# Optimization experiments

Hardware: AMD Instinct MI355X
Metric: run time of the kernel (lower is better)

The kernel has to match this reference:

```python
import jax, jax.numpy as jnp
import numpy as np

N, T, DM = 8192, 32, 128   # nodes, patches, d_model (d_in = T*DM = 4096)
M, NNZ = 1024, 131072      # hyperedges, incidences
EPS = 1e-5
SLOPE = 0.2


def _bn(x, g, b, axes):
    # BatchNorm with batch statistics (training-mode math, eval dropout)
    m = jnp.mean(x, axis=axes, keepdims=True)
    v = jnp.var(x, axis=axes, keepdims=True)
    return (x - m) / jnp.sqrt(v + EPS) * g + b


def _hconv(x, he_attr, he_n, he_e, W, att, bias, heads):
    # PyG HypergraphConv, use_attention=True, attention_mode='node', concat=False
    out = W.shape[1] // heads
    xt = (x @ W).reshape(N, heads, out)          # [N, H, F]
    et = (he_attr @ W).reshape(M, heads, out)    # [M, H, F]
    xi = xt[he_n]                                # [nnz, H, F] gather node feats
    ej = et[he_e]                                # [nnz, H, F] gather edge feats
    alpha = jnp.sum(jnp.concatenate([xi, ej], axis=-1) * att, axis=-1)  # [nnz, H]
    alpha = jax.nn.leaky_relu(alpha, SLOPE)
    # segment softmax grouped by hyperedge (attention_mode='node')
    amax = jax.ops.segment_max(alpha, he_e, num_segments=M)
    ex = jnp.exp(alpha - amax[he_e])
    alpha = ex / jax.ops.segment_sum(ex, he_e, num_segments=M)[he_e]
    # degree normalizers (hyperedge_weight == 1)
    ones = jnp.ones((NNZ,), x.dtype)
    Dn = jax.ops.segment_sum(ones, he_n, num_segments=N)
    Dinv = jnp.where(Dn > 0, 1.0 / Dn, 0.0)
    Bm = jax.ops.segment_sum(ones, he_e, num_segments=M)
    Binv = jnp.where(Bm > 0, 1.0 / Bm, 0.0)
    # node -> edge, then edge -> node message passing
    eo = jax.ops.segment_sum(alpha[:, :, None] * Binv[he_e][:, None, None] * xi,
                             he_e, num_segments=M)                     # [M, H, F]
    no = jax.ops.segment_sum(alpha[:, :, None] * Dinv[he_n][:, None, None] * eo[he_e],
                             he_n, num_segments=N)                     # [N, H, F]
    return no.mean(axis=1) + bias  # concat=False -> mean over heads


def setup_inputs() -> dict:
    key = jax.random.key(0)
    ks = jax.random.split(key, 16)
    d_in = T * DM
    s = 0.02
    inp = {
        "x": jax.random.normal(ks[0], (N, T, DM), jnp.float32),
        "he_nodes": jax.random.randint(ks[1], (NNZ,), 0, N),
        "he_edges": jax.random.randint(ks[2], (NNZ,), 0, M),
        "W1": jax.random.normal(ks[3], (d_in, DM), jnp.float32) * s,
        "b1": jnp.zeros((DM,), jnp.float32),
        "g1": jnp.ones((DM,), jnp.float32), "be1": jnp.zeros((DM,), jnp.float32),
        "Wh1": jax.random.normal(ks[4], (DM, 4 * DM), jnp.float32) * s,
        "att1": jax.random.normal(ks[5], (1, 4, 2 * DM), jnp.float32) * s,
        "bh1": jnp.zeros((DM,), jnp.float32),
        "g2": jnp.ones((DM,), jnp.float32), "be2": jnp.zeros((DM,), jnp.float32),
        "Wh2": jax.random.normal(ks[6], (DM, DM), jnp.float32) * s,
        "att2": jax.random.normal(ks[7], (1, 1, 2 * DM), jnp.float32) * s,
        "bh2": jnp.zeros((DM,), jnp.float32),
        "g3": jnp.ones((DM,), jnp.float32), "be3": jnp.zeros((DM,), jnp.float32),
        "W3": jax.random.normal(ks[8], (DM, d_in), jnp.float32) * s,
        "b3": jnp.zeros((d_in,), jnp.float32),
        "g4": jnp.ones((DM,), jnp.float32), "be4": jnp.zeros((DM,), jnp.float32),
    }
    return inp


def reference(x, he_nodes, he_edges, W1, b1, g1, be1, Wh1, att1, bh1,
              g2, be2, Wh2, att2, bh2, g3, be3, W3, b3, g4, be4):
    src = x
    h = x.reshape(N, T * DM)
    h = jax.nn.leaky_relu(h @ W1 + b1, SLOPE)
    h = _bn(h, g1, be1, 0)
    # hyperedge_attr = incidence^T @ h  (== to_dense_adj(...).T @ h)
    he_attr = jax.ops.segment_sum(h[he_nodes], he_edges, num_segments=M)
    h = h + _hconv(h, he_attr, he_nodes, he_edges, Wh1, att1, bh1, 4)
    h = _bn(h, g2, be2, 0)
    he_attr = jax.ops.segment_sum(h[he_nodes], he_edges, num_segments=M)
    h = h + _hconv(h, he_attr, he_nodes, he_edges, Wh2, att2, bh2, 1)
    h = _bn(h, g3, be3, 0)
    h = jax.nn.leaky_relu(h @ W3 + b3, SLOPE)
    h = src + h.reshape(N, T, DM)
    h = _bn(h, g4, be4, (0, 1))  # BN over channel DM, stats over (N, T)
    return h
```

## Files before the change

kernel.cpp:

```cpp
#include <hip/hip_runtime.h>
#include <hip/hip_bf16.h>
#include <math.h>

#define NN   8192
#define TT   32
#define DIN  4096
#define MME  1024
#define NNZK 131072
#define EPSV 1e-5f
#define MALL (NN + MME)

typedef __attribute__((ext_vector_type(8))) short bf16x8;
typedef __attribute__((ext_vector_type(4))) float f32x4;

__device__ __forceinline__ float lrelu(float v){ return v > 0.f ? v : 0.2f*v; }
__device__ __forceinline__ short f2b(float f){
    union { __hip_bfloat16 h; short s; } u; u.h = __float2bfloat16(f); return u.s;
}

__global__ void zero_i(int* p, int n){ int i = blockIdx.x*256 + threadIdx.x; if (i < n) p[i] = 0; }
__global__ void zero_f(float* p, int n){ int i = blockIdx.x*256 + threadIdx.x; if (i < n) p[i] = 0.f; }
__global__ void copy_i(const int* a, int* b, int n){ int i = blockIdx.x*256 + threadIdx.x; if (i < n) b[i] = a[i]; }

__global__ void count_seg(const int* __restrict__ he_n, const int* __restrict__ he_e,
                          int* __restrict__ ncnt, int* __restrict__ ecnt){
    int k = blockIdx.x*256 + threadIdx.x;
    if (k < NNZK){ atomicAdd(&ecnt[he_e[k]], 1); atomicAdd(&ncnt[he_n[k]], 1); }
}

__global__ void scan_excl(const int* __restrict__ cnt, int* __restrict__ off, int n){
    __shared__ int buf[1024];
    __shared__ int carry;
    int t = threadIdx.x;
    if (t == 0) carry = 0;
    __syncthreads();
    for (int base = 0; base < n; base += 1024){
        int i = base + t;
        int v = (i < n) ? cnt[i] : 0;
        buf[t] = v; __syncthreads();
        for (int s = 1; s < 1024; s <<= 1){
            int tmp = (t >= s) ? buf[t - s] : 0;
            __syncthreads();
            buf[t] += tmp;
            __syncthreads();
        }
        if (i < n) off[i] = carry + buf[t] - v;
        __syncthreads();
        if (t == 1023) carry += buf[1023];
        __syncthreads();
    }
    if (t == 0) off[n] = carry;
}

__global__ void fill_perm(const int* __restrict__ seg, int* __restrict__ cur, int* __restrict__ perm){
    int k = blockIdx.x*256 + threadIdx.x;
    if (k < NNZK){ int p = atomicAdd(&cur[seg[k]], 1); perm[p] = k; }
}

__global__ void wconv_t(const float* __restrict__ W, __hip_bfloat16* __restrict__ BT, int K, int N){
    __shared__ float tile[32][33];
    int k0 = blockIdx.y*32, n0 = blockIdx.x*32;
    int tx = threadIdx.x & 31, ty = threadIdx.x >> 5;
    for (int i = ty; i < 32; i += 8) tile[i][tx] = W[(size_t)(k0+i)*N + n0+tx];
    __syncthreads();
    for (int i = ty; i < 32; i += 8)
        BT[(size_t)(n0+i)*K + k0 + tx] = __float2bfloat16(tile[tx][i]);
}

#define SWZ(b) ((b) ^ ((((b) >> 6) & 7) << 4))

template<int EPI>
__global__ __launch_bounds__(256) void gemm_mfma(
    const float* __restrict__ A, const __hip_bfloat16* __restrict__ BT,
    float* __restrict__ C, const float* __restrict__ bias, const float* __restrict__ add,
    float* __restrict__ slots, int M, int N, int K, int kchunk)
{
    __shared__ f32x4 AsRaw[512];
    __shared__ f32x4 BsRaw[512];
    char* As = (char*)AsRaw;
    char* Bs = (char*)BsRaw;
    const int tid = threadIdx.x;
    const int lane = tid & 63;
    const int w = tid >> 6;
    const int m0 = blockIdx.y << 7, n0 = blockIdx.x << 7;
    const int kz = blockIdx.z * kchunk;
    const int wr = (w >> 1) << 6, wc = (w & 1) << 6;

    const int s0 = tid, s1 = tid + 256;
    const int r0 = s0 >> 2, k0b = (s0 & 3) << 3;
    const int r1 = s1 >> 2, k1b = (s1 & 3) << 3;
    const float* pA0 = A + (size_t)(m0 + r0)*K + kz + k0b;
    const float* pA1 = A + (size_t)(m0 + r1)*K + kz + k1b;
    const __hip_bfloat16* pB0 = BT + (size_t)(n0 + r0)*K + kz + k0b;
    const __hip_bfloat16* pB1 = BT + (size_t)(n0 + r1)*K + kz + k1b;
    const int wo0 = SWZ(s0 << 4), wo1 = SWZ(s1 << 4);

    int raOff[4], rbOff[4];
#pragma unroll
    for (int f = 0; f < 4; f++){
        int rowA = wr + f*16 + (lane & 15);
        raOff[f] = SWZ(rowA*64 + ((lane >> 4) << 4));
        int rowB = wc + f*16 + (lane & 15);
        rbOff[f] = SWZ(rowB*64 + ((lane >> 4) << 4));
    }

    f32x4 acc[4][4] = {};

    float4 a0l = *(const float4*)pA0, a0h = *(const float4*)(pA0+4);
    float4 a1l = *(const float4*)pA1, a1h = *(const float4*)(pA1+4);
    bf16x8 b0 = *(const bf16x8*)pB0, b1 = *(const bf16x8*)pB1;

    const int nsteps = kchunk >> 5;
    for (int ks = 0; ks < nsteps; ks++){
        bf16x8 va0, va1;
        va0[0]=f2b(a0l.x); va0[1]=f2b(a0l.y); va0[2]=f2b(a0l.z); va0[3]=f2b(a0l.w);
        va0[4]=f2b(a0h.x); va0[5]=f2b(a0h.y); va0[6]=f2b(a0h.z); va0[7]=f2b(a0h.w);
        va1[0]=f2b(a1l.x); va1[1]=f2b(a1l.y); va1[2]=f2b(a1l.z); va1[3]=f2b(a1l.w);
        va1[4]=f2b(a1h.x); va1[5]=f2b(a1h.y); va1[6]=f2b(a1h.z); va1[7]=f2b(a1h.w);
        __syncthreads();
        *(bf16x8*)(As + wo0) = va0;
        *(bf16x8*)(As + wo1) = va1;
        *(bf16x8*)(Bs + wo0) = b0;
        *(bf16x8*)(Bs + wo1) = b1;
        __syncthreads();
        if (ks + 1 < nsteps){
            pA0 += 32; pA1 += 32; pB0 += 32; pB1 += 32;
            a0l = *(const float4*)pA0; a0h = *(const float4*)(pA0+4);
            a1l = *(const float4*)pA1; a1h = *(const float4*)(pA1+4);
            b0 = *(const bf16x8*)pB0;  b1 = *(const bf16x8*)pB1;
        }
        bf16x8 af[4], bfr[4];
#pragma unroll
        for (int f = 0; f < 4; f++){
            af[f]  = *(const bf16x8*)(As + raOff[f]);
            bfr[f] = *(const bf16x8*)(Bs + rbOff[f]);
        }
#pragma unroll
        for (int mf = 0; mf < 4; mf++)
#pragma unroll
            for (int nf = 0; nf < 4; nf++)
                acc[mf][nf] = __builtin_amdgcn_mfma_f32_16x16x32_bf16(af[mf], bfr[nf], acc[mf][nf], 0, 0, 0);
    }

    if (EPI == 2){
        __shared__ float sS[128], sQ[128];
        if (tid < 128){ sS[tid] = 0.f; sQ[tid] = 0.f; }
        __syncthreads();
#pragma unroll
        for (int nf = 0; nf < 4; nf++){
            int lc = wc + nf*16 + (lane & 15);
            int col = n0 + lc;
            float bv = bias[col];
            float s = 0.f, q = 0.f;
#pragma unroll
            for (int mf = 0; mf < 4; mf++){
#pragma unroll
                for (int r = 0; r < 4; r++){
                    int row = m0 + wr + mf*16 + ((lane >> 4) << 2) + r;
                    float v = acc[mf][nf][r] + bv;
                    v = lrelu(v);
                    v += add[(size_t)row*N + col];
                    C[(size_t)row*N + col] = v;
                    s += v; q += v*v;
                }
            }
            atomicAdd(&sS[lc], s);
            atomicAdd(&sQ[lc], q);
        }
        __syncthreads();
        if (tid < 128){
            atomicAdd(&slots[blockIdx.x*256 + tid], sS[tid]);
            atomicAdd(&slots[blockIdx.x*256 + 128 + tid], sQ[tid]);
        }
    } else {
        float* Cz = C + (size_t)blockIdx.z * ((size_t)M * (size_t)N);
#pragma unroll
        for (int mf = 0; mf < 4; mf++){
#pragma unroll
            for (int nf = 0; nf < 4; nf++){
                int col = n0 + wc + nf*16 + (lane & 15);
#pragma unroll
                for (int r = 0; r < 4; r++){
                    int row = m0 + wr + mf*16 + ((lane >> 4) << 2) + r;
                    Cz[(size_t)row*N + col] = acc[mf][nf][r];
                }
            }
        }
    }
}

__global__ void reduce8s(const float* __restrict__ part, const float* __restrict__ bias,
                         float* __restrict__ out, int nf4, int parts, float* __restrict__ slots){
    int tid = threadIdx.x;
    int i = blockIdx.x*256 + tid;
    float4 s = ((const float4*)part)[i];
    for (int z = 1; z < parts; z++){
        float4 p = ((const float4*)part)[(size_t)z*nf4 + i];
        s.x += p.x; s.y += p.y; s.z += p.z; s.w += p.w;
    }
    int c0 = (i & 31) << 2;
    s.x = lrelu(s.x + bias[c0+0]); s.y = lrelu(s.y + bias[c0+1]);
    s.z = lrelu(s.z + bias[c0+2]); s.w = lrelu(s.w + bias[c0+3]);
    ((float4*)out)[i] = s;
    __shared__ float S[128], Q[128];
    if (tid < 128){ S[tid] = 0.f; Q[tid] = 0.f; }
    __syncthreads();
    atomicAdd(&S[c0+0], s.x); atomicAdd(&Q[c0+0], s.x*s.x);
    atomicAdd(&S[c0+1], s.y); atomicAdd(&Q[c0+1], s.y*s.y);
    atomicAdd(&S[c0+2], s.z); atomicAdd(&Q[c0+2], s.z*s.z);
    atomicAdd(&S[c0+3], s.w); atomicAdd(&Q[c0+3], s.w*s.w);
    __syncthreads();
    if (tid < 128){
        int slot = blockIdx.x & 31;
        atomicAdd(&slots[slot*256 + tid], S[tid]);
        atomicAdd(&slots[slot*256 + 128 + tid], Q[tid]);
    }
}

__global__ void bn_stats_v2(const float* __restrict__ x, float* __restrict__ slots, int rows){
    int cg = threadIdx.x & 31, rg = threadIdx.x >> 5;
    float4 s = {0,0,0,0}, q = {0,0,0,0};
    for (int r = blockIdx.x*8 + rg; r < rows; r += gridDim.x*8){
        float4 v = ((const float4*)x)[(size_t)r*32 + cg];
        s.x += v.x; q.x += v.x*v.x;
        s.y += v.y; q.y += v.y*v.y;
        s.z += v.z; q.z += v.z*v.z;
        s.w += v.w; q.w += v.w*v.w;
    }
    __shared__ float S[128], Q[128];
    if (threadIdx.x < 128){ S[threadIdx.x] = 0.f; Q[threadIdx.x] = 0.f; }
    __syncthreads();
    int c0 = cg << 2;
    atomicAdd(&S[c0+0], s.x); atomicAdd(&Q[c0+0], q.x);
    atomicAdd(&S[c0+1], s.y); atomicAdd(&Q[c0+1], q.y);
    atomicAdd(&S[c0+2], s.z); atomicAdd(&Q[c0+2], q.z);
    atomicAdd(&S[c0+3], s.w); atomicAdd(&Q[c0+3], q.w);
    __syncthreads();
    if (threadIdx.x < 128){
        int slot = blockIdx.x & 31;
        atomicAdd(&slots[slot*256 + threadIdx.x], S[threadIdx.x]);
        atomicAdd(&slots[slot*256 + 128 + threadIdx.x], Q[threadIdx.x]);
    }
}

__global__ void bn_finalize2(const float* __restrict__ slots, int nslots,
                             const float* __restrict__ g, const float* __restrict__ b,
                             float invR, float* __restrict__ coef){
    int c = threadIdx.x;
    float s = 0.f, q = 0.f;
    for (int k = 0; k < nslots; k++){ s += slots[k*256 + c]; q += slots[k*256 + 128 + c]; }
    float m = s*invR;
    float v = q*invR - m*m;
    float sc = g[c]*rsqrtf(v + EPSV);
    coef[c] = sc;
    coef[128 + c] = b[c] - m*sc;
}

__global__ void bn_apply4(float4* __restrict__ x, const float* __restrict__ coef, size_t n4){
    size_t i = (size_t)blockIdx.x*blockDim.x + threadIdx.x;
    size_t stride = (size_t)gridDim.x*blockDim.x;
    for (; i < n4; i += stride){
        int c0 = (int)(i & 31) * 4;
        float4 v = x[i];
        v.x = v.x*coef[c0+0] + coef[128+c0+0];
        v.y = v.y*coef[c0+1] + coef[128+c0+1];
        v.z = v.z*coef[c0+2] + coef[128+c0+2];
        v.w = v.w*coef[c0+3] + coef[128+c0+3];
        x[i] = v;
    }
}

__global__ void seg_sum_edge(const int* __restrict__ eoff, const int* __restrict__ eperm,
                             const int* __restrict__ he_n, const float* __restrict__ h,
                             float* __restrict__ out){
    int m = blockIdx.x, c = threadIdx.x;
    int s0 = eoff[m], cnt = eoff[m+1] - s0;
    __shared__ int sn[128];
    float acc = 0.f;
    for (int base = 0; base < cnt; base += 128){
        int i = base + c;
        if (i < cnt) sn[c] = he_n[eperm[s0+i]];
        __syncthreads();
        int lim = min(128, cnt - base);
        for (int j = 0; j < lim; j++) acc += h[(size_t)sn[j]*128 + c];
        __syncthreads();
    }
    out[(size_t)m*128 + c] = acc;
}

template<int H>
__global__ void row_att(const float* __restrict__ xt, const float* __restrict__ att,
                        int aoff, float* __restrict__ out){
    int n = blockIdx.x, lane = threadIdx.x;
#pragma unroll
    for (int h = 0; h < H; h++){
        const float* xr = xt + (size_t)n*(H*128) + h*128;
        const float* ar = att + h*256 + aoff;
        float s = xr[lane]*ar[lane] + xr[lane+64]*ar[lane+64];
        for (int d = 32; d > 0; d >>= 1) s += __shfl_down(s, d);
        if (lane == 0) out[n*H + h] = s;
    }
}

template<int H>
__global__ void seg_softmax(const int* __restrict__ eoff, const int* __restrict__ eperm,
                            const int* __restrict__ he_n,
                            const float* __restrict__ ax, const float* __restrict__ ae,
                            float* __restrict__ alpha){
    int m = blockIdx.x, t = threadIdx.x;
    int s0 = eoff[m], cnt = eoff[m+1] - s0;
    if (cnt == 0) return;
    __shared__ float red[128];
    float aeh[H];
#pragma unroll
    for (int h = 0; h < H; h++) aeh[h] = ae[m*H + h];
    float lmax[H];
#pragma unroll
    for (int h = 0; h < H; h++) lmax[h] = -1e30f;
    for (int i = t; i < cnt; i += 128){
        int k = eperm[s0+i]; int n = he_n[k];
#pragma unroll
        for (int h = 0; h < H; h++){
            float v = lrelu(ax[n*H + h] + aeh[h]);
            alpha[(size_t)k*H + h] = v;
            lmax[h] = fmaxf(lmax[h], v);
        }
    }
    float gmax[H];
#pragma unroll
    for (int h = 0; h < H; h++){
        red[t] = lmax[h]; __syncthreads();
        for (int s = 64; s > 0; s >>= 1){ if (t < s) red[t] = fmaxf(red[t], red[t+s]); __syncthreads(); }
        gmax[h] = red[0]; __syncthreads();
    }
    float lsum[H];
#pragma unroll
    for (int h = 0; h < H; h++) lsum[h] = 0.f;
    for (int i = t; i < cnt; i += 128){
        int k = eperm[s0+i];
#pragma unroll
        for (int h = 0; h < H; h++){
            float ex = __expf(alpha[(size_t)k*H + h] - gmax[h]);
            alpha[(size_t)k*H + h] = ex;
            lsum[h] += ex;
        }
    }
    float ginv[H];
#pragma unroll
    for (int h = 0; h < H; h++){
        red[t] = lsum[h]; __syncthreads();
        for (int s = 64; s > 0; s >>= 1){ if (t < s) red[t] += red[t+s]; __syncthreads(); }
        ginv[h] = 1.f/red[0]; __syncthreads();
    }
    for (int i = t; i < cnt; i += 128){
        int k = eperm[s0+i];
#pragma unroll
        for (int h = 0; h < H; h++) alpha[(size_t)k*H + h] *= ginv[h];
    }
}

__global__ void seg_eo4(const int* __restrict__ eoff, const int* __restrict__ eperm,
                        const int* __restrict__ he_n,
                        const float* __restrict__ alpha, const float* __restrict__ xt,
                        float* __restrict__ eo){
    int m = blockIdx.x;
    int c = threadIdx.x & 127, hb = threadIdx.x >> 7;
    int s0 = eoff[m], cnt = eoff[m+1] - s0;
    __shared__ int sn[128];
    __shared__ float sa[128][4];
    float acc0 = 0.f, acc1 = 0.f;
    for (int base = 0; base < cnt; base += 128){
        int i = base + threadIdx.x;
        if (threadIdx.x < 128 && i < cnt){
            int k = eperm[s0+i];
            sn[threadIdx.x] = he_n[k];
#pragma unroll
            for (int h = 0; h < 4; h++) sa[threadIdx.x][h] = alpha[(size_t)k*4 + h];
        }
        __syncthreads();
        int lim = min(128, cnt - base);
        for (int j = 0; j < lim; j++){
            const float* xr = xt + (size_t)sn[j]*512;
            acc0 += sa[j][hb]   * xr[hb*128 + c];
            acc1 += sa[j][hb+2] * xr[(hb+2)*128 + c];
        }
        __syncthreads();
    }
    float binv = cnt > 0 ? 1.f/(float)cnt : 0.f;
    eo[(size_t)m*512 + hb*128 + c]     = acc0*binv;
    eo[(size_t)m*512 + (hb+2)*128 + c] = acc1*binv;
}

__global__ void seg_eo1(const int* __restrict__ eoff, const int* __restrict__ eperm,
                        const int* __restrict__ he_n,
                        const float* __restrict__ alpha, const float* __restrict__ xt,
                        float* __restrict__ eo){
    int m = blockIdx.x, c = threadIdx.x;
    int s0 = eoff[m], cnt = eoff[m+1] - s0;
    __shared__ int sn[128];
    __shared__ float sa[128];
    float acc = 0.f;
    for (int base = 0; base < cnt; base += 128){
        int i = base + c;
        if (i < cnt){
            int k = eperm[s0+i];
            sn[c] = he_n[k];
            sa[c] = alpha[k];
        }
        __syncthreads();
        int lim = min(128, cnt - base);
        for (int j = 0; j < lim; j++) acc += sa[j]*xt[(size_t)sn[j]*128 + c];
        __syncthreads();
    }
    float binv = cnt > 0 ? 1.f/(float)cnt : 0.f;
    eo[(size_t)m*128 + c] = acc*binv;
}

template<int H>
__global__ void seg_node_out(const int* __restrict__ noff, const int* __restrict__ nperm,
                             const int* __restrict__ he_e,
                             const float* __restrict__ alpha, const float* __restrict__ eo,
                             const float* __restrict__ hin, const float* __restrict__ bias,
                             float* __restrict__ hout){
    int n = blockIdx.x, c = threadIdx.x;
    int s0 = noff[n], cnt = noff[n+1] - s0;
    float acc = 0.f;
    for (int i = 0; i < cnt; i++){
        int k = nperm[s0+i]; int e = he_e[k];
        const float* er = eo + (size_t)e*(128*H);
#pragma unroll
        for (int h = 0; h < H; h++) acc += alpha[(size_t)k*H + h]*er[h*128 + c];
    }
    float dinv = cnt > 0 ? 1.f/((float)cnt*(float)H) : 0.f;
    hout[(size_t)n*128 + c] = hin[(size_t)n*128 + c] + bias[c] + acc*dinv;
}

extern "C" void kernel_launch(void* const* d_in, const int* in_sizes, int n_in,
                              void* d_out, int out_size, void* d_ws, size_t ws_size,
                              hipStream_t stream){
    const float* x    = (const float*)d_in[0];
    const int*   he_n = (const int*)  d_in[1];
    const int*   he_e = (const int*)  d_in[2];
    const float* W1   = (const float*)d_in[3];
    const float* b1   = (const float*)d_in[4];
    const float* g1   = (const float*)d_in[5];
    const float* be1  = (const float*)d_in[6];
    const float* Wh1  = (const float*)d_in[7];
    const float* att1 = (const float*)d_in[8];
    const float* bh1  = (const float*)d_in[9];
    const float* g2   = (const float*)d_in[10];
    const float* be2  = (const float*)d_in[11];
    const float* Wh2  = (const float*)d_in[12];
    const float* att2 = (const float*)d_in[13];
    const float* bh2  = (const float*)d_in[14];
    const float* g3   = (const float*)d_in[15];
    const float* be3  = (const float*)d_in[16];
    const float* W3   = (const float*)d_in[17];
    const float* b3   = (const float*)d_in[18];
    const float* g4   = (const float*)d_in[19];
    const float* be4  = (const float*)d_in[20];
    float* out = (float*)d_out;

    char* ws = (char*)d_ws;
    size_t off = 0;
    auto alloc = [&](size_t bytes)->char*{ char* p = ws + off; off += (bytes + 255) & ~(size_t)255; return p; };

    float* hall1  = (float*)alloc((size_t)MALL*128*4);
    float* hall2  = (float*)alloc((size_t)MALL*128*4);
    float* h3     = (float*)alloc((size_t)NN*128*4);
    float* xt1    = (float*)alloc((size_t)MALL*512*4);
    float* xt2    = (float*)alloc((size_t)MALL*128*4);
    float* eo     = (float*)alloc((size_t)MME*512*4);
    float* alpha  = (float*)alloc((size_t)NNZK*4*4);
    float* ax     = (float*)alloc((size_t)NN*4*4);
    float* ae     = (float*)alloc((size_t)MME*4*4);
    float* slots  = (float*)alloc((size_t)32*256*4);
    float* coef   = (float*)alloc(256*4);
    float* part   = (float*)alloc((size_t)8*NN*128*4);
    __hip_bfloat16* W1T  = (__hip_bfloat16*)alloc((size_t)128*DIN*2);
    __hip_bfloat16* Wh1T = (__hip_bfloat16*)alloc((size_t)512*128*2);
    __hip_bfloat16* Wh2T = (__hip_bfloat16*)alloc((size_t)128*128*2);
    __hip_bfloat16* W3T  = (__hip_bfloat16*)alloc((size_t)DIN*128*2);
    int* ecnt  = (int*)alloc(MME*4);
    int* eoffb = (int*)alloc((MME+1)*4);
    int* ecur  = (int*)alloc(MME*4);
    int* ncnt  = (int*)alloc(NN*4);
    int* noffb = (int*)alloc((NN+1)*4);
    int* ncur  = (int*)alloc(NN*4);
    int* eperm = (int*)alloc((size_t)NNZK*4);
    int* nperm = (int*)alloc((size_t)NNZK*4);

    zero_i<<<(MME+255)/256, 256, 0, stream>>>(ecnt, MME);
    zero_i<<<(NN+255)/256, 256, 0, stream>>>(ncnt, NN);
    count_seg<<<NNZK/256, 256, 0, stream>>>(he_n, he_e, ncnt, ecnt);
    scan_excl<<<1, 1024, 0, stream>>>(ecnt, eoffb, MME);
    scan_excl<<<1, 1024, 0, stream>>>(ncnt, noffb, NN);
    copy_i<<<(MME+255)/256, 256, 0, stream>>>(eoffb, ecur, MME);
    copy_i<<<(NN+255)/256, 256, 0, stream>>>(noffb, ncur, NN);
    fill_perm<<<NNZK/256, 256, 0, stream>>>(he_e, ecur, eperm);
    fill_perm<<<NNZK/256, 256, 0, stream>>>(he_n, ncur, nperm);

    wconv_t<<<dim3(128/32, DIN/32), 256, 0, stream>>>(W1,  W1T,  DIN, 128);
    wconv_t<<<dim3(512/32, 128/32), 256, 0, stream>>>(Wh1, Wh1T, 128, 512);
    wconv_t<<<dim3(128/32, 128/32), 256, 0, stream>>>(Wh2, Wh2T, 128, 128);
    wconv_t<<<dim3(DIN/32, 128/32), 256, 0, stream>>>(W3,  W3T,  128, DIN);

    gemm_mfma<0><<<dim3(1, NN/128, 8), 256, 0, stream>>>(x, W1T, part, nullptr, nullptr, nullptr, NN, 128, DIN, DIN/8);
    zero_f<<<32, 256, 0, stream>>>(slots, 32*256);
    reduce8s<<<NN*128/4/256, 256, 0, stream>>>(part, b1, hall1, NN*128/4, 8, slots);
    bn_finalize2<<<1, 128, 0, stream>>>(slots, 32, g1, be1, 1.f/NN, coef);
    bn_apply4<<<1024, 256, 0, stream>>>((float4*)hall1, coef, (size_t)NN*32);

    seg_sum_edge<<<MME, 128, 0, stream>>>(eoffb, eperm, he_n, hall1, hall1 + (size_t)NN*128);
    gemm_mfma<0><<<dim3(512/128, MALL/128, 1), 256, 0, stream>>>(hall1, Wh1T, xt1, nullptr, nullptr, nullptr, MALL, 512, 128, 128);
    row_att<4><<<NN, 64, 0, stream>>>(xt1, att1, 0, ax);
    row_att<4><<<MME, 64, 0, stream>>>(xt1 + (size_t)NN*512, att1, 128, ae);
    seg_softmax<4><<<MME, 128, 0, stream>>>(eoffb, eperm, he_n, ax, ae, alpha);
    seg_eo4<<<MME, 256, 0, stream>>>(eoffb, eperm, he_n, alpha, xt1, eo);
    seg_node_out<4><<<NN, 128, 0, stream>>>(noffb, nperm, he_e, alpha, eo, hall1, bh1, hall2);
    zero_f<<<32, 256, 0, stream>>>(slots, 32*256);
    bn_stats_v2<<<256, 256, 0, stream>>>(hall2, slots, NN);
    bn_finalize2<<<1, 128, 0, stream>>>(slots, 32, g2, be2, 1.f/NN, coef);
    bn_apply4<<<1024, 256, 0, stream>>>((float4*)hall2, coef, (size_t)NN*32);

    seg_sum_edge<<<MME, 128, 0, stream>>>(eoffb, eperm, he_n, hall2, hall2 + (size_t)NN*128);
    gemm_mfma<0><<<dim3(1, MALL/128, 1), 256, 0, stream>>>(hall2, Wh2T, xt2, nullptr, nullptr, nullptr, MALL, 128, 128, 128);
    row_att<1><<<NN, 64, 0, stream>>>(xt2, att2, 0, ax);
    row_att<1><<<MME, 64, 0, stream>>>(xt2 + (size_t)NN*128, att2, 128, ae);
    seg_softmax<1><<<MME, 128, 0, stream>>>(eoffb, eperm, he_n, ax, ae, alpha);
    seg_eo1<<<MME, 128, 0, stream>>>(eoffb, eperm, he_n, alpha, xt2, eo);
    seg_node_out<1><<<NN, 128, 0, stream>>>(noffb, nperm, he_e, alpha, eo, hall2, bh2, h3);
    zero_f<<<32, 256, 0, stream>>>(slots, 32*256);
    bn_stats_v2<<<256, 256, 0, stream>>>(h3, slots, NN);
    bn_finalize2<<<1, 128, 0, stream>>>(slots, 32, g3, be3, 1.f/NN, coef);
    bn_apply4<<<1024, 256, 0, stream>>>((float4*)h3, coef, (size_t)NN*32);

    zero_f<<<32, 256, 0, stream>>>(slots, 32*256);
    gemm_mfma<2><<<dim3(DIN/128, NN/128, 1), 256, 0, stream>>>(h3, W3T, out, b3, x, slots, NN, DIN, 128, 128);
    bn_finalize2<<<1, 128, 0, stream>>>(slots, 32, g4, be4, 1.f/((float)NN*TT), coef);
    bn_apply4<<<4096, 256, 0, stream>>>((float4*)out, coef, (size_t)NN*TT*32);
}
```

Measured before the change: 532.9 us.

## Recompute final GEMM to fuse BatchNorm apply instead of storing intermediate

The final W3 GEMM now runs twice. A stats-only pass computes the per-channel sums without writing the 8192x4096 output. A second pass recomputes the GEMM and applies bias, leaky ReLU, the residual add and the BN affine in its epilogue before a single vectorized store. This removes the full-size output write, the read-back and the rewrite done by the separate bn_apply pass, at the cost of doing the GEMM and the residual read twice. The operands are swapped in a new gemm_nt kernel so each lane holds four consecutive columns for float4 stores, and the two zero kernels are merged into one.

```diff
diff --git a/kernel.cpp b/kernel.cpp
--- a/kernel.cpp
+++ b/kernel.cpp
@@ -69,10 +69,110 @@
 
 #define SWZ(b) ((b) ^ ((((b) >> 6) & 7) << 4))
 
-template<int EPI>
-__global__ __launch_bounds__(256) void gemm_mfma(
+template<int MODE>
+__global__ __launch_bounds__(256) void gemm_nt(
+    const float* __restrict__ Aact, const __hip_bfloat16* __restrict__ Bwt,
+    float* __restrict__ C, const float* __restrict__ bias, const float* __restrict__ add,
+    const float* __restrict__ coef, int M, int N, int K, int kchunk)
+{
+    __shared__ f32x4 WsRaw[512];
+    __shared__ f32x4 XsRaw[512];
+    char* Ws = (char*)WsRaw;
+    char* Xs = (char*)XsRaw;
+    const int tid = threadIdx.x;
+    const int lane = tid & 63;
+    const int w = tid >> 6;
+    const int m0 = blockIdx.y << 7, n0 = blockIdx.x << 7;
+    const int kz = blockIdx.z * kchunk;
+    const int wN = (w >> 1) << 6, wM = (w & 1) << 6;
+
+    const int s0 = tid, s1 = tid + 256;
+    const int r0 = s0 >> 2, k0b = (s0 & 3) << 3;
+    const int r1 = s1 >> 2, k1b = (s1 & 3) << 3;
+    const float* pX0 = Aact + (size_t)(m0 + r0)*K + kz + k0b;
+    const float* pX1 = Aact + (size_t)(m0 + r1)*K + kz + k1b;
+    const __hip_bfloat16* pW0 = Bwt + (size_t)(n0 + r0)*K + kz + k0b;
+    const __hip_bfloat16* pW1 = Bwt + (size_t)(n0 + r1)*K + kz + k1b;
+    const int wo0 = SWZ(s0 << 4), wo1 = SWZ(s1 << 4);
+
+    int rwOff[4], rxOff[4];
+#pragma unroll
+    for (int f = 0; f < 4; f++){
+        rwOff[f] = SWZ((wN + f*16 + (lane & 15))*64 + ((lane >> 4) << 4));
+        rxOff[f] = SWZ((wM + f*16 + (lane & 15))*64 + ((lane >> 4) << 4));
+    }
+
+    f32x4 acc[4][4] = {};
+
+    float4 x0l = *(const float4*)pX0, x0h = *(const float4*)(pX0+4);
+    float4 x1l = *(const float4*)pX1, x1h = *(const float4*)(pX1+4);
+    bf16x8 w0 = *(const bf16x8*)pW0, w1 = *(const bf16x8*)pW1;
+
+    const int nsteps = kchunk >> 5;
+    for (int ks = 0; ks < nsteps; ks++){
+        bf16x8 vx0, vx1;
+        vx0[0]=f2b(x0l.x); vx0[1]=f2b(x0l.y); vx0[2]=f2b(x0l.z); vx0[3]=f2b(x0l.w);
+        vx0[4]=f2b(x0h.x); vx0[5]=f2b(x0h.y); vx0[6]=f2b(x0h.z); vx0[7]=f2b(x0h.w);
+        vx1[0]=f2b(x1l.x); vx1[1]=f2b(x1l.y); vx1[2]=f2b(x1l.z); vx1[3]=f2b(x1l.w);
+        vx1[4]=f2b(x1h.x); vx1[5]=f2b(x1h.y); vx1[6]=f2b(x1h.z); vx1[7]=f2b(x1h.w);
+        __syncthreads();
+        *(bf16x8*)(Xs + wo0) = vx0;
+        *(bf16x8*)(Xs + wo1) = vx1;
+        *(bf16x8*)(Ws + wo0) = w0;
+        *(bf16x8*)(Ws + wo1) = w1;
+        __syncthreads();
+        if (ks + 1 < nsteps){
+            pX0 += 32; pX1 += 32; pW0 += 32; pW1 += 32;
+            x0l = *(const float4*)pX0; x0h = *(const float4*)(pX0+4);
+            x1l = *(const float4*)pX1; x1h = *(const float4*)(pX1+4);
+            w0 = *(const bf16x8*)pW0;  w1 = *(const bf16x8*)pW1;
+        }
+        bf16x8 wf[4], xf[4];
+#pragma unroll
+        for (int f = 0; f < 4; f++){
+            wf[f] = *(const bf16x8*)(Ws + rwOff[f]);
+            xf[f] = *(const bf16x8*)(Xs + rxOff[f]);
+        }
+#pragma unroll
+        for (int i = 0; i < 4; i++)
+#pragma unroll
+            for (int j = 0; j < 4; j++)
+                acc[i][j] = __builtin_amdgcn_mfma_f32_16x16x32_bf16(wf[i], xf[j], acc[i][j], 0, 0, 0);
+    }
+
+    const int mc = wM + (lane & 15);
+    const int ncb = wN + ((lane >> 4) << 2);
+    float* Cz = (MODE == 0) ? C + (size_t)blockIdx.z * ((size_t)M * (size_t)N) : C;
+#pragma unroll
+    for (int j = 0; j < 4; j++){
+        int row = m0 + mc + j*16;
+#pragma unroll
+        for (int i = 0; i < 4; i++){
+            int col = n0 + ncb + i*16;
+            f32x4 v = acc[i][j];
+            if (MODE == 1){
+                float4 b4 = *(const float4*)&bias[col];
+                v[0] = lrelu(v[0] + b4.x);
+                v[1] = lrelu(v[1] + b4.y);
+                v[2] = lrelu(v[2] + b4.z);
+                v[3] = lrelu(v[3] + b4.w);
+                float4 a4 = *(const float4*)&add[(size_t)row*N + col];
+                int ch = (ncb + i*16) & 127;
+                float4 sc = *(const float4*)&coef[ch];
+                float4 sh = *(const float4*)&coef[128 + ch];
+                v[0] = (v[0] + a4.x)*sc.x + sh.x;
+                v[1] = (v[1] + a4.y)*sc.y + sh.y;
+                v[2] = (v[2] + a4.z)*sc.z + sh.z;
+                v[3] = (v[3] + a4.w)*sc.w + sh.w;
+            }
+            *(float4*)&Cz[(size_t)row*N + col] = *(float4*)&v;
+        }
+    }
+}
+
+__global__ __launch_bounds__(256) void gemm_stats(
     const float* __restrict__ A, const __hip_bfloat16* __restrict__ BT,
-    float* __restrict__ C, const float* __restrict__ bias, const float* __restrict__ add,
+    const float* __restrict__ bias, const float* __restrict__ add,
     float* __restrict__ slots, int M, int N, int K, int kchunk)
 {
     __shared__ f32x4 AsRaw[512];
@@ -83,25 +183,22 @@
     const int lane = tid & 63;
     const int w = tid >> 6;
     const int m0 = blockIdx.y << 7, n0 = blockIdx.x << 7;
-    const int kz = blockIdx.z * kchunk;
     const int wr = (w >> 1) << 6, wc = (w & 1) << 6;
 
     const int s0 = tid, s1 = tid + 256;
     const int r0 = s0 >> 2, k0b = (s0 & 3) << 3;
     const int r1 = s1 >> 2, k1b = (s1 & 3) << 3;
-    const float* pA0 = A + (size_t)(m0 + r0)*K + kz + k0b;
-    const float* pA1 = A + (size_t)(m0 + r1)*K + kz + k1b;
-    const __hip_bfloat16* pB0 = BT + (size_t)(n0 + r0)*K + kz + k0b;
-    const __hip_bfloat16* pB1 = BT + (size_t)(n0 + r1)*K + kz + k1b;
+    const float* pA0 = A + (size_t)(m0 + r0)*K + k0b;
+    const float* pA1 = A + (size_t)(m0 + r1)*K + k1b;
+    const __hip_bfloat16* pB0 = BT + (size_t)(n0 + r0)*K + k0b;
+    const __hip_bfloat16* pB1 = BT + (size_t)(n0 + r1)*K + k1b;
     const int wo0 = SWZ(s0 << 4), wo1 = SWZ(s1 << 4);
 
     int raOff[4], rbOff[4];
 #pragma unroll
     for (int f = 0; f < 4; f++){
-        int rowA = wr + f*16 + (lane & 15);
-        raOff[f] = SWZ(rowA*64 + ((lane >> 4) << 4));
-        int rowB = wc + f*16 + (lane & 15);
-        rbOff[f] = SWZ(rowB*64 + ((lane >> 4) << 4));
+        raOff[f] = SWZ((wr + f*16 + (lane & 15))*64 + ((lane >> 4) << 4));
+        rbOff[f] = SWZ((wc + f*16 + (lane & 15))*64 + ((lane >> 4) << 4));
     }
 
     f32x4 acc[4][4] = {};
@@ -142,50 +239,31 @@
                 acc[mf][nf] = __builtin_amdgcn_mfma_f32_16x16x32_bf16(af[mf], bfr[nf], acc[mf][nf], 0, 0, 0);
     }
 
-    if (EPI == 2){
-        __shared__ float sS[128], sQ[128];
-        if (tid < 128){ sS[tid] = 0.f; sQ[tid] = 0.f; }
-        __syncthreads();
-#pragma unroll
-        for (int nf = 0; nf < 4; nf++){
-            int lc = wc + nf*16 + (lane & 15);
-            int col = n0 + lc;
-            float bv = bias[col];
-            float s = 0.f, q = 0.f;
-#pragma unroll
-            for (int mf = 0; mf < 4; mf++){
-#pragma unroll
-                for (int r = 0; r < 4; r++){
-                    int row = m0 + wr + mf*16 + ((lane >> 4) << 2) + r;
-                    float v = acc[mf][nf][r] + bv;
-                    v = lrelu(v);
-                    v += add[(size_t)row*N + col];
-                    C[(size_t)row*N + col] = v;
-                    s += v; q += v*v;
-                }
+    __shared__ float sS[128], sQ[128];
+    if (tid < 128){ sS[tid] = 0.f; sQ[tid] = 0.f; }
+    __syncthreads();
+#pragma unroll
+    for (int nf = 0; nf < 4; nf++){
+        int lc = wc + nf*16 + (lane & 15);
+        int col = n0 + lc;
+        float bv = bias[col];
+        float s = 0.f, q = 0.f;
+#pragma unroll
+        for (int mf = 0; mf < 4; mf++){
+#pragma unroll
+            for (int r = 0; r < 4; r++){
+                int row = m0 + wr + mf*16 + ((lane >> 4) << 2) + r;
+                float v = lrelu(acc[mf][nf][r] + bv) + add[(size_t)row*N + col];
+                s += v; q += v*v;
             }
-            atomicAdd(&sS[lc], s);
-            atomicAdd(&sQ[lc], q);
-        }
-        __syncthreads();
-        if (tid < 128){
-            atomicAdd(&slots[blockIdx.x*256 + tid], sS[tid]);
-            atomicAdd(&slots[blockIdx.x*256 + 128 + tid], sQ[tid]);
-        }
-    } else {
-        float* Cz = C + (size_t)blockIdx.z * ((size_t)M * (size_t)N);
-#pragma unroll
-        for (int mf = 0; mf < 4; mf++){
-#pragma unroll
-            for (int nf = 0; nf < 4; nf++){
-                int col = n0 + wc + nf*16 + (lane & 15);
-#pragma unroll
-                for (int r = 0; r < 4; r++){
-                    int row = m0 + wr + mf*16 + ((lane >> 4) << 2) + r;
-                    Cz[(size_t)row*N + col] = acc[mf][nf][r];
-                }
-            }
-        }
+        }
+        atomicAdd(&sS[lc & 127], s);
+        atomicAdd(&sQ[lc & 127], q);
+    }
+    __syncthreads();
+    if (tid < 128){
+        atomicAdd(&slots[(blockIdx.x & 31)*256 + tid], sS[tid]);
+        atomicAdd(&slots[(blockIdx.x & 31)*256 + 128 + tid], sQ[tid]);
     }
 }
 
@@ -482,16 +560,15 @@
     __hip_bfloat16* Wh2T = (__hip_bfloat16*)alloc((size_t)128*128*2);
     __hip_bfloat16* W3T  = (__hip_bfloat16*)alloc((size_t)DIN*128*2);
     int* ecnt  = (int*)alloc(MME*4);
+    int* ncnt  = (int*)alloc(NN*4);
     int* eoffb = (int*)alloc((MME+1)*4);
     int* ecur  = (int*)alloc(MME*4);
-    int* ncnt  = (int*)alloc(NN*4);
     int* noffb = (int*)alloc((NN+1)*4);
     int* ncur  = (int*)alloc(NN*4);
     int* eperm = (int*)alloc((size_t)NNZK*4);
     int* nperm = (int*)alloc((size_t)NNZK*4);
 
-    zero_i<<<(MME+255)/256, 256, 0, stream>>>(ecnt, MME);
-    zero_i<<<(NN+255)/256, 256, 0, stream>>>(ncnt, NN);
+    zero_i<<<(MME+NN+255)/256, 256, 0, stream>>>(ecnt, MME+NN);
     count_seg<<<NNZK/256, 256, 0, stream>>>(he_n, he_e, ncnt, ecnt);
     scan_excl<<<1, 1024, 0, stream>>>(ecnt, eoffb, MME);
     scan_excl<<<1, 1024, 0, stream>>>(ncnt, noffb, NN);
@@ -505,14 +582,14 @@
     wconv_t<<<dim3(128/32, 128/32), 256, 0, stream>>>(Wh2, Wh2T, 128, 128);
     wconv_t<<<dim3(DIN/32, 128/32), 256, 0, stream>>>(W3,  W3T,  128, DIN);
 
-    gemm_mfma<0><<<dim3(1, NN/128, 8), 256, 0, stream>>>(x, W1T, part, nullptr, nullptr, nullptr, NN, 128, DIN, DIN/8);
+    gemm_nt<0><<<dim3(1, NN/128, 8), 256, 0, stream>>>(x, W1T, part, nullptr, nullptr, nullptr, NN, 128, DIN, DIN/8);
     zero_f<<<32, 256, 0, stream>>>(slots, 32*256);
     reduce8s<<<NN*128/4/256, 256, 0, stream>>>(part, b1, hall1, NN*128/4, 8, slots);
     bn_finalize2<<<1, 128, 0, stream>>>(slots, 32, g1, be1, 1.f/NN, coef);
     bn_apply4<<<1024, 256, 0, stream>>>((float4*)hall1, coef, (size_t)NN*32);
 
     seg_sum_edge<<<MME, 128, 0, stream>>>(eoffb, eperm, he_n, hall1, hall1 + (size_t)NN*128);
-    gemm_mfma<0><<<dim3(512/128, MALL/128, 1), 256, 0, stream>>>(hall1, Wh1T, xt1, nullptr, nullptr, nullptr, MALL, 512, 128, 128);
+    gemm_nt<0><<<dim3(512/128, MALL/128, 1), 256, 0, stream>>>(hall1, Wh1T, xt1, nullptr, nullptr, nullptr, MALL, 512, 128, 128);
     row_att<4><<<NN, 64, 0, stream>>>(xt1, att1, 0, ax);
     row_att<4><<<MME, 64, 0, stream>>>(xt1 + (size_t)NN*512, att1, 128, ae);
     seg_softmax<4><<<MME, 128, 0, stream>>>(eoffb, eperm, he_n, ax, ae, alpha);
@@ -524,7 +601,7 @@
     bn_apply4<<<1024, 256, 0, stream>>>((float4*)hall2, coef, (size_t)NN*32);
 
     seg_sum_edge<<<MME, 128, 0, stream>>>(eoffb, eperm, he_n, hall2, hall2 + (size_t)NN*128);
-    gemm_mfma<0><<<dim3(1, MALL/128, 1), 256, 0, stream>>>(hall2, Wh2T, xt2, nullptr, nullptr, nullptr, MALL, 128, 128, 128);
+    gemm_nt<0><<<dim3(1, MALL/128, 1), 256, 0, stream>>>(hall2, Wh2T, xt2, nullptr, nullptr, nullptr, MALL, 128, 128, 128);
     row_att<1><<<NN, 64, 0, stream>>>(xt2, att2, 0, ax);
     row_att<1><<<MME, 64, 0, stream>>>(xt2 + (size_t)NN*128, att2, 128, ae);
     seg_softmax<1><<<MME, 128, 0, stream>>>(eoffb, eperm, he_n, ax, ae, alpha);
@@ -536,7 +613,7 @@
     bn_apply4<<<1024, 256, 0, stream>>>((float4*)h3, coef, (size_t)NN*32);
 
     zero_f<<<32, 256, 0, stream>>>(slots, 32*256);
-    gemm_mfma<2><<<dim3(DIN/128, NN/128, 1), 256, 0, stream>>>(h3, W3T, out, b3, x, slots, NN, DIN, 128, 128);
+    gemm_stats<<<dim3(DIN/128, NN/128), 256, 0, stream>>>(h3, W3T, b3, x, slots, NN, DIN, 128, 128);
     bn_finalize2<<<1, 128, 0, stream>>>(slots, 32, g4, be4, 1.f/((float)NN*TT), coef);
-    bn_apply4<<<4096, 256, 0, stream>>>((float4*)out, coef, (size_t)NN*TT*32);
-}
+    gemm_nt<1><<<dim3(DIN/128, NN/128, 1), 256, 0, stream>>>(h3, W3T, out, b3, x, coef, NN, DIN, 128, 128);
+}
```

After: 526.7 us. About the same (-1.2%).
